# Kernel tuning notes

Measured on AMD Instinct MI355X. Metric: run time of the kernel, lower is better.

The kernel has to match this reference:

```python
import jax, jax.numpy as jnp
import numpy as np

B, T, C = 8, 2048, 1024
E = 8            # num_experts (= world_size in the original)
K = 2            # top-k
CAP_FACTOR = 1.25
CAPACITY = int(T / E * CAP_FACTOR)  # 320, per (expert, batch-row)
DFF = 4 * C


def setup_inputs() -> dict:
    key = jax.random.key(0)
    ks = jax.random.split(key, 4)
    x = jax.random.normal(ks[0], (B, T, C), dtype=jnp.float32)
    Wg = jax.random.normal(ks[1], (C, E), dtype=jnp.float32) * (C ** -0.5)
    bg = jnp.zeros((E,), dtype=jnp.float32)
    W1 = jax.random.normal(ks[2], (E, C, DFF), dtype=jnp.float32) * (C ** -0.5)
    b1 = jnp.zeros((E, DFF), dtype=jnp.float32)
    W2 = jax.random.normal(ks[3], (E, DFF, C), dtype=jnp.float32) * (DFF ** -0.5)
    b2 = jnp.zeros((E, C), dtype=jnp.float32)
    return {"x": x, "Wg": Wg, "bg": bg, "W1": W1, "b1": b1, "W2": W2, "b2": b2}


def reference(x, Wg, bg, W1, b1, W2, b2):
    # Router: linear + softmax, then top-k gating
    probs = jax.nn.softmax(jnp.einsum('btc,ce->bte', x, Wg) + bg, axis=-1)  # [B,T,E]
    topk_p, topk_e = jax.lax.top_k(probs, K)                               # [B,T,K]

    S = T * K  # one "assignment" per (token, k-slot), row-major (t, k) order
    e_flat = topk_e.reshape(B, S)                      # expert id per assignment
    p_flat = topk_p.reshape(B, S)

    # Position of each assignment within its (batch-row, expert) group,
    # ordered by token position then k-slot (matches nonzero() row-major order).
    onehot = (e_flat[..., None] == jnp.arange(E)).astype(jnp.int32)        # [B,S,E]
    pos_all = jnp.cumsum(onehot, axis=1) - 1                                # [B,S,E]
    pos = jnp.take_along_axis(pos_all, e_flat[..., None], axis=2)[..., 0]   # [B,S]
    keep = pos < CAPACITY                               # overflow tokens are dropped

    # Dispatch tokens into padded per-(expert,row) buffers: [E,B,CAPACITY,C]
    x_rep = jnp.repeat(x, K, axis=1)                    # [B,S,C], assignment order
    b_idx = jnp.broadcast_to(jnp.arange(B)[:, None], (B, S))
    pos_scat = jnp.where(keep, pos, CAPACITY)           # out-of-range -> dropped
    dispatch = jnp.zeros((E, B, CAPACITY, C), dtype=x.dtype)
    dispatch = dispatch.at[e_flat, b_idx, pos_scat].set(x_rep, mode='drop')

    # Grouped expert FFN (padding rows are zeros; their outputs are never read back)
    h = jax.nn.relu(jnp.einsum('ebsc,ech->ebsh', dispatch, W1) + b1[:, None, None, :])
    y = jnp.einsum('ebsh,ehc->ebsc', h, W2) + b2[:, None, None, :]

    # Combine: gather back, scale by gate prob (dropped tokens -> padding_val 0)
    gathered = y[e_flat, b_idx, jnp.clip(pos, 0, CAPACITY - 1)]             # [B,S,C]
    out = gathered * jnp.where(keep, p_flat, 0.0)[..., None]
    return out.reshape(B, T, K, C).sum(axis=2)          # sum over k assignments
```

## Files before the change

### kernel.cpp

```cpp
#include <hip/hip_runtime.h>
#include <stdint.h>

#define B_ 8
#define T_ 2048
#define C_ 1024
#define E_ 8
#define K_ 2
#define CAP_ 320
#define DFF_ 4096
#define S_ (T_*K_)
#define NTOK (B_*T_)
#define ROWS_PER_E (B_*CAP_)

typedef __attribute__((ext_vector_type(8))) short short8;
typedef __attribute__((ext_vector_type(4))) float floatx4;

__device__ __forceinline__ unsigned short f2bf(float f) {
  union { float f; unsigned u; } v; v.f = f;
  unsigned r = v.u + 0x7fffu + ((v.u >> 16) & 1u);
  return (unsigned short)(r >> 16);
}
__device__ __forceinline__ float bf2f(unsigned short h) {
  union { unsigned u; float f; } v; v.u = ((unsigned)h) << 16;
  return v.f;
}

#define GLOAD16(g, l) __builtin_amdgcn_global_load_lds( \
    (const __attribute__((address_space(1))) void*)(g), \
    (__attribute__((address_space(3))) void*)(l), 16, 0, 0)

__global__ void router_kernel(const float* __restrict__ x, const float* __restrict__ Wg,
                              const float* __restrict__ bg,
                              int* __restrict__ topk_e, float* __restrict__ topk_p)
{
  int token = (int)((blockIdx.x * blockDim.x + threadIdx.x) >> 6);
  int lane = threadIdx.x & 63;
  if (token >= NTOK) return;
  const float* xr = x + (size_t)token * C_;
  double acc[E_];
  #pragma unroll
  for (int e = 0; e < E_; ++e) acc[e] = 0.0;
  for (int c = lane; c < C_; c += 64) {
    double xv = (double)xr[c];
    const float4* w4 = (const float4*)(Wg + (size_t)c * E_);
    float4 wa = w4[0], wb = w4[1];
    acc[0] += xv * (double)wa.x; acc[1] += xv * (double)wa.y;
    acc[2] += xv * (double)wa.z; acc[3] += xv * (double)wa.w;
    acc[4] += xv * (double)wb.x; acc[5] += xv * (double)wb.y;
    acc[6] += xv * (double)wb.z; acc[7] += xv * (double)wb.w;
  }
  #pragma unroll
  for (int off = 32; off; off >>= 1) {
    #pragma unroll
    for (int e = 0; e < E_; ++e) acc[e] += __shfl_down(acc[e], off, 64);
  }
  if (lane == 0) {
    double lg[E_];
    double mx = -1e300;
    #pragma unroll
    for (int e = 0; e < E_; ++e) { lg[e] = acc[e] + (double)bg[e]; mx = fmax(mx, lg[e]); }
    double se = 0.0, pr[E_];
    #pragma unroll
    for (int e = 0; e < E_; ++e) { pr[e] = exp(lg[e] - mx); se += pr[e]; }
    #pragma unroll
    for (int e = 0; e < E_; ++e) pr[e] /= se;
    int e0 = 0;
    #pragma unroll
    for (int e = 1; e < E_; ++e) if (pr[e] > pr[e0]) e0 = e;
    int e1 = -1;
    #pragma unroll
    for (int e = 0; e < E_; ++e) {
      if (e == e0) continue;
      if (e1 < 0 || pr[e] > pr[e1]) e1 = e;
    }
    topk_e[token*2+0] = e0; topk_p[token*2+0] = (float)pr[e0];
    topk_e[token*2+1] = e1; topk_p[token*2+1] = (float)pr[e1];
  }
}

__global__ void scan_kernel(const int* __restrict__ topk_e,
                            int* __restrict__ pos_arr,
                            int* __restrict__ slot_src,
                            int* __restrict__ counts)
{
  const int b = blockIdx.x;
  const int tid = threadIdx.x;
  const int PT = S_ / 256;
  __shared__ int cnt[256][E_];
  int e_loc[16];
  int local[E_];
  #pragma unroll
  for (int e = 0; e < E_; ++e) local[e] = 0;
  const int* te = topk_e + (size_t)b * S_;
  for (int j = 0; j < PT; ++j) {
    int e = te[tid*PT + j];
    e_loc[j] = e;
    local[e]++;
  }
  #pragma unroll
  for (int e = 0; e < E_; ++e) cnt[tid][e] = local[e];
  __syncthreads();
  if (tid < E_) {
    int run = 0;
    for (int i = 0; i < 256; ++i) { int v = cnt[i][tid]; cnt[i][tid] = run; run += v; }
    counts[tid*B_ + b] = run;
  }
  __syncthreads();
  int base[E_];
  #pragma unroll
  for (int e = 0; e < E_; ++e) base[e] = cnt[tid][e];
  for (int j = 0; j < PT; ++j) {
    int e = e_loc[j];
    int p = base[e]++;
    int s = tid*PT + j;
    if (p < CAP_) {
      pos_arr[(size_t)b*S_ + s] = p;
      slot_src[((size_t)e*B_ + b)*CAP_ + p] = s >> 1;
    } else {
      pos_arr[(size_t)b*S_ + s] = -1;
    }
  }
}

__global__ void transpose_conv_kernel(const float* __restrict__ in, unsigned short* __restrict__ out,
                                      int R, int Cc)
{
  __shared__ float tile[64][33];
  const int e = blockIdx.z;
  const float* ine = in + (size_t)e * R * Cc;
  unsigned short* oute = out + (size_t)e * R * Cc;
  const int c0 = blockIdx.x * 32, r0 = blockIdx.y * 64;
  const int tx = threadIdx.x & 7, ty = threadIdx.x >> 3;
  #pragma unroll
  for (int p = 0; p < 2; ++p) {
    const int rr = p*32 + ty;
    float4 v = *(const float4*)(ine + (size_t)(r0 + rr) * Cc + c0 + tx*4);
    tile[rr][tx*4+0] = v.x; tile[rr][tx*4+1] = v.y;
    tile[rr][tx*4+2] = v.z; tile[rr][tx*4+3] = v.w;
  }
  __syncthreads();
  short8 s;
  #pragma unroll
  for (int j = 0; j < 8; ++j) s[j] = (short)f2bf(tile[tx*8+j][ty]);
  *(short8*)(oute + (size_t)(c0 + ty) * R + r0 + tx*8) = s;
}

__global__ void dispatch_kernel(const float* __restrict__ x, const int* __restrict__ slot_src,
                                const int* __restrict__ counts, unsigned short* __restrict__ Xd,
                                int e_base, int nexp)
{
  int row = (int)((blockIdx.x * blockDim.x + threadIdx.x) >> 6);
  int lane = threadIdx.x & 63;
  int total = nexp * B_ * CAP_;
  if (row >= total) return;
  int el = row / (B_*CAP_);
  int rem = row - el*(B_*CAP_);
  int b = rem / CAP_, slot = rem - b*CAP_;
  int eg = e_base + el;
  int cnt = counts[eg*B_ + b]; if (cnt > CAP_) cnt = CAP_;
  unsigned short* orow = Xd + (size_t)row * C_;
  if (slot < cnt) {
    int t = slot_src[((size_t)eg*B_ + b)*CAP_ + slot];
    const float4* xr = (const float4*)(x + ((size_t)b*T_ + t)*C_);
    #pragma unroll
    for (int i = 0; i < C_/256; ++i) {
      float4 v = xr[i*64 + lane];
      ushort4 o;
      o.x = f2bf(v.x); o.y = f2bf(v.y); o.z = f2bf(v.z); o.w = f2bf(v.w);
      ((ushort4*)orow)[i*64 + lane] = o;
    }
  } else {
    ushort4 z; z.x = z.y = z.z = z.w = 0;
    #pragma unroll
    for (int i = 0; i < C_/256; ++i) ((ushort4*)orow)[i*64 + lane] = z;
  }
}

template<int RELU>
__global__ __launch_bounds__(256, 3) void gemm128_kernel(
    const unsigned short* __restrict__ A,
    const unsigned short* __restrict__ BT,
    const float* __restrict__ bias,
    unsigned short* __restrict__ Out0,
    unsigned short* __restrict__ Out1,
    int M, int N, int Kfull, int klen, int tilesPerSplit, int nwg)
{
  __shared__ __align__(16) unsigned short lds[3*8192];
  const int NT = N >> 7, MT = M >> 7;
  const int bid = blockIdx.x;
  const int wg = (bid & 7) * (nwg >> 3) + (bid >> 3);
  const int sp  = wg / tilesPerSplit;
  const int wgr = wg - sp * tilesPerSplit;
  const int e  = wgr / (MT*NT);
  const int r2 = wgr - e*(MT*NT);
  const int mt = r2 / NT, nt = r2 - mt*NT;
  const int k0 = sp * klen;
  const unsigned short* Ae = A + (size_t)e * M * Kfull;
  const unsigned short* Be = BT + (size_t)e * N * Kfull;
  const float* be = bias ? (bias + (size_t)e * N) : nullptr;
  unsigned short* Oe = (sp == 0 ? Out0 : Out1) + (size_t)e * M * N;
  const int m0 = mt*128, n0 = nt*128;

  const int tid = threadIdx.x, lane = tid & 63, w = tid >> 6;
  const int wr = w >> 1, wc = w & 1;

  floatx4 acc[4][4];
  #pragma unroll
  for (int i = 0; i < 4; ++i)
    #pragma unroll
    for (int j = 0; j < 4; ++j) acc[i][j] = (floatx4){0.f, 0.f, 0.f, 0.f};

  const int c0 = tid, c1 = 256 + tid;
  const int sr0 = c0 >> 2, sr1 = c1 >> 2;
  const int sq0 = ((c0 & 3)*8) ^ (((sr0 >> 1) & 3) << 3);
  const int sq1 = ((c1 & 3)*8) ^ (((sr1 >> 1) & 3) << 3);
  const unsigned short* gA0 = Ae + (size_t)(m0 + sr0)*Kfull + k0 + sq0;
  const unsigned short* gA1 = Ae + (size_t)(m0 + sr1)*Kfull + k0 + sq1;
  const unsigned short* gB0 = Be + (size_t)(n0 + sr0)*Kfull + k0 + sq0;
  const unsigned short* gB1 = Be + (size_t)(n0 + sr1)*Kfull + k0 + sq1;
  const int la0 = w*512, la1 = 2048 + w*512;
  const int lb0 = 4096 + w*512, lb1 = 4096 + 2048 + w*512;

  const int fr = lane & 15, kq = lane >> 4;
  const int aRow = wr*64 + fr;
  const int bRow = wc*64 + fr;
  const int aOff = aRow*32 + ((kq*8) ^ (((aRow >> 1) & 3) << 3));
  const int bOff = 4096 + bRow*32 + ((kq*8) ^ (((bRow >> 1) & 3) << 3));

  const int nk = klen >> 5;

#define STAGE(t, slot) do { \
    GLOAD16(gA0 + (size_t)(t)*32, lds + (slot)*8192 + la0); \
    GLOAD16(gA1 + (size_t)(t)*32, lds + (slot)*8192 + la1); \
    GLOAD16(gB0 + (size_t)(t)*32, lds + (slot)*8192 + lb0); \
    GLOAD16(gB1 + (size_t)(t)*32, lds + (slot)*8192 + lb1); } while(0)

  STAGE(0, 0); STAGE(1, 1);
  asm volatile("s_waitcnt vmcnt(4)" ::: "memory");
  __builtin_amdgcn_s_barrier();

  for (int t = 0; t < nk; ++t) {
    const int slot = t % 3;
    const int ps   = (t + 2) % 3;
    const unsigned short* sT = lds + slot*8192;

    short8 af[4], bf[4];
    #pragma unroll
    for (int mf = 0; mf < 4; ++mf) af[mf] = *(const short8*)(sT + aOff + mf*512);
    #pragma unroll
    for (int nf = 0; nf < 4; ++nf) bf[nf] = *(const short8*)(sT + bOff + nf*512);
    if (t + 2 < nk) STAGE(t+2, ps);

    #pragma unroll
    for (int mf = 0; mf < 4; ++mf)
      #pragma unroll
      for (int nf = 0; nf < 4; ++nf)
        acc[mf][nf] = __builtin_amdgcn_mfma_f32_16x16x32_bf16(af[mf], bf[nf], acc[mf][nf], 0, 0, 0);

    if (t + 1 < nk) {
      asm volatile("s_waitcnt lgkmcnt(0)" ::: "memory");
      if (t + 2 < nk) asm volatile("s_waitcnt vmcnt(4)" ::: "memory");
      else            asm volatile("s_waitcnt vmcnt(0)" ::: "memory");
      __builtin_amdgcn_s_barrier();
    }
  }
#undef STAGE

  const int col = lane & 15, rbase = (lane >> 4) * 4;
  #pragma unroll
  for (int mf = 0; mf < 4; ++mf) {
    const int gr0 = m0 + wr*64 + mf*16 + rbase;
    #pragma unroll
    for (int nf = 0; nf < 4; ++nf) {
      const int gc = n0 + wc*64 + nf*16 + col;
      const float bv = be ? be[gc] : 0.f;
      #pragma unroll
      for (int r = 0; r < 4; ++r) {
        float v = acc[mf][nf][r] + bv;
        if (RELU) v = fmaxf(v, 0.f);
        Oe[(size_t)(gr0 + r)*N + gc] = f2bf(v);
      }
    }
  }
}

__global__ void combine_kernel(const unsigned short* __restrict__ Y0,
                               const unsigned short* __restrict__ Y1,
                               const float* __restrict__ b2c,
                               const int* __restrict__ topk_e, const float* __restrict__ topk_p,
                               const int* __restrict__ pos_arr, float* __restrict__ out)
{
  int token = (int)((blockIdx.x * blockDim.x + threadIdx.x) >> 6);
  int lane = threadIdx.x & 63;
  if (token >= NTOK) return;
  int b = token / T_, t = token - b*T_;
  int s0 = b*S_ + t*2;
  float acc[16];
  #pragma unroll
  for (int i = 0; i < 16; ++i) acc[i] = 0.f;
  #pragma unroll
  for (int k = 0; k < 2; ++k) {
    int pos = pos_arr[s0 + k];
    if (pos < 0) continue;
    int e = topk_e[s0 + k];
    float p = topk_p[s0 + k];
    size_t rowoff = (((size_t)e*B_ + b)*CAP_ + pos) * C_;
    const unsigned short* yr0 = Y0 + rowoff;
    const unsigned short* yr1 = Y1 ? (Y1 + rowoff) : nullptr;
    const float* bb = b2c ? (b2c + (size_t)e * C_) : nullptr;
    #pragma unroll
    for (int i = 0; i < 4; ++i) {
      ushort4 v = ((const ushort4*)yr0)[i*64 + lane];
      float s0v = bf2f(v.x), s1v = bf2f(v.y), s2v = bf2f(v.z), s3v = bf2f(v.w);
      if (yr1) {
        ushort4 u = ((const ushort4*)yr1)[i*64 + lane];
        s0v += bf2f(u.x); s1v += bf2f(u.y); s2v += bf2f(u.z); s3v += bf2f(u.w);
      }
      if (bb) {
        float4 bv = ((const float4*)bb)[i*64 + lane];
        s0v += bv.x; s1v += bv.y; s2v += bv.z; s3v += bv.w;
      }
      acc[i*4+0] += p * s0v;
      acc[i*4+1] += p * s1v;
      acc[i*4+2] += p * s2v;
      acc[i*4+3] += p * s3v;
    }
  }
  float4* orow = (float4*)(out + (size_t)token * C_);
  #pragma unroll
  for (int i = 0; i < 4; ++i) {
    float4 o;
    o.x = acc[i*4+0]; o.y = acc[i*4+1]; o.z = acc[i*4+2]; o.w = acc[i*4+3];
    orow[i*64 + lane] = o;
  }
}

extern "C" void kernel_launch(void* const* d_in, const int* in_sizes, int n_in,
                              void* d_out, int out_size, void* d_ws, size_t ws_size,
                              hipStream_t stream)
{
  const float* x  = (const float*)d_in[0];
  const float* Wg = (const float*)d_in[1];
  const float* bg = (const float*)d_in[2];
  const float* W1 = (const float*)d_in[3];
  const float* b1 = (const float*)d_in[4];
  const float* W2 = (const float*)d_in[5];
  const float* b2 = (const float*)d_in[6];
  float* out = (float*)d_out;

  char* ws = (char*)d_ws;
  size_t off = 0;
  auto alloc = [&](size_t bytes) -> char* {
    char* p = ws + off;
    off = (off + bytes + 255) & ~(size_t)255;
    return p;
  };
  int*   topk_e  = (int*)  alloc((size_t)NTOK * K_ * 4);
  float* topk_p  = (float*)alloc((size_t)NTOK * K_ * 4);
  int*   pos_arr = (int*)  alloc((size_t)B_ * S_ * 4);
  int*   slot_src= (int*)  alloc((size_t)E_ * B_ * CAP_ * 4);
  int*   counts  = (int*)  alloc((size_t)E_ * B_ * 4);
  unsigned short* Ybuf = (unsigned short*)alloc((size_t)E_ * ROWS_PER_E * C_ * 2);
  size_t fixed = off;
  const size_t perE = (size_t)C_ * DFF_ * 2
                    + (size_t)ROWS_PER_E * C_ * 2
                    + (size_t)ROWS_PER_E * DFF_ * 2
                    + 3 * 256;
  int k = 8;
  while (k > 1 && fixed + (size_t)k * perE > ws_size) k >>= 1;
  unsigned short* Wt = (unsigned short*)alloc((size_t)k * C_ * DFF_ * 2);
  unsigned short* Xd = (unsigned short*)alloc((size_t)k * ROWS_PER_E * C_ * 2);
  unsigned short* Hb = (unsigned short*)alloc((size_t)k * ROWS_PER_E * DFF_ * 2);

  router_kernel<<<NTOK/4, 256, 0, stream>>>(x, Wg, bg, topk_e, topk_p);
  scan_kernel<<<B_, 256, 0, stream>>>(topk_e, pos_arr, slot_src, counts);

  const bool splitK2 = (k == 8);

  for (int eb = 0; eb < E_; eb += k) {
    transpose_conv_kernel<<<dim3(DFF_/32, C_/64, k), 256, 0, stream>>>(
        W1 + (size_t)eb * C_ * DFF_, Wt, C_, DFF_);
    dispatch_kernel<<<(k * ROWS_PER_E) / 4, 256, 0, stream>>>(x, slot_src, counts, Xd, eb, k);
    {
      int tiles = k * (ROWS_PER_E/128) * (DFF_/128);
      gemm128_kernel<1><<<tiles, 256, 0, stream>>>(
          Xd, Wt, b1 + (size_t)eb * DFF_, Hb, Hb, ROWS_PER_E, DFF_, C_, C_, tiles, tiles);
    }
    transpose_conv_kernel<<<dim3(C_/32, DFF_/64, k), 256, 0, stream>>>(
        W2 + (size_t)eb * DFF_ * C_, Wt, DFF_, C_);
    {
      int tiles = k * (ROWS_PER_E/128) * (C_/128);
      if (splitK2) {
        gemm128_kernel<0><<<2*tiles, 256, 0, stream>>>(
            Hb, Wt, nullptr, Ybuf, Xd, ROWS_PER_E, C_, DFF_, DFF_/2, tiles, 2*tiles);
      } else {
        gemm128_kernel<0><<<tiles, 256, 0, stream>>>(
            Hb, Wt, b2 + (size_t)eb * C_, Ybuf + (size_t)eb * ROWS_PER_E * C_,
            Ybuf + (size_t)eb * ROWS_PER_E * C_, ROWS_PER_E, C_, DFF_, DFF_, tiles, tiles);
      }
    }
  }

  combine_kernel<<<NTOK/4, 256, 0, stream>>>(
      Ybuf, splitK2 ? Xd : nullptr, splitK2 ? b2 : nullptr,
      topk_e, topk_p, pos_arr, out);
}
```

Baseline: 630.6 us.

## Replace 128x128 GEMM with 256x256 tile, 8-wave kernel and interleaved staging

Replaces the 128x128, 4-wave, triple-buffered GEMM with a 256x256 tile using 8 waves (each computing 128x64), a 64-wide K step split into half-tiles, and A/B loads staggered between four MFMA phases with barriers and s_setprio. Larger tiles raise arithmetic intensity and cut global/LDS traffic per FLOP, and the interleaved schedule aims to overlap loads with MFMA. In exchange it uses 128KB LDS per block (one block per CU) and launches far fewer workgroups: 256x256 tiles give 10x16=160 per expert for GEMM1 and 10x4=40 per expert for GEMM2, which may underfill the CUs for GEMM2. It also adds many barriers per iteration.

```diff
diff --git a/kernel.cpp b/kernel.cpp
--- a/kernel.cpp
+++ b/kernel.cpp
@@ -29,6 +29,8 @@
     (const __attribute__((address_space(1))) void*)(g), \
     (__attribute__((address_space(3))) void*)(l), 16, 0, 0)
 
+#define BARRIER() asm volatile("s_barrier" ::: "memory")
+
 __global__ void router_kernel(const float* __restrict__ x, const float* __restrict__ Wg,
                               const float* __restrict__ bg,
                               int* __restrict__ topk_e, float* __restrict__ topk_p)
@@ -79,8 +81,7 @@
 }
 
 __global__ void scan_kernel(const int* __restrict__ topk_e,
-                            int* __restrict__ pos_arr,
-                            int* __restrict__ slot_src,
+                            int* __restrict__ pos_arr, int* __restrict__ slot_src,
                             int* __restrict__ counts)
 {
   const int b = blockIdx.x;
@@ -177,7 +178,7 @@
 }
 
 template<int RELU>
-__global__ __launch_bounds__(256, 3) void gemm128_kernel(
+__global__ __launch_bounds__(512) void gemm256_kernel(
     const unsigned short* __restrict__ A,
     const unsigned short* __restrict__ BT,
     const float* __restrict__ bias,
@@ -185,8 +186,8 @@
     unsigned short* __restrict__ Out1,
     int M, int N, int Kfull, int klen, int tilesPerSplit, int nwg)
 {
-  __shared__ __align__(16) unsigned short lds[3*8192];
-  const int NT = N >> 7, MT = M >> 7;
+  __shared__ __align__(16) unsigned short lds[65536];
+  const int NT = N >> 8, MT = M >> 8;
   const int bid = blockIdx.x;
   const int wg = (bid & 7) * (nwg >> 3) + (bid >> 3);
   const int sp  = wg / tilesPerSplit;
@@ -199,77 +200,123 @@
   const unsigned short* Be = BT + (size_t)e * N * Kfull;
   const float* be = bias ? (bias + (size_t)e * N) : nullptr;
   unsigned short* Oe = (sp == 0 ? Out0 : Out1) + (size_t)e * M * N;
-  const int m0 = mt*128, n0 = nt*128;
+  const int m0 = mt*256, n0 = nt*256;
 
   const int tid = threadIdx.x, lane = tid & 63, w = tid >> 6;
-  const int wr = w >> 1, wc = w & 1;
-
-  floatx4 acc[4][4];
-  #pragma unroll
-  for (int i = 0; i < 4; ++i)
+  const int wr = w >> 2, wc = w & 3;
+
+  floatx4 acc[8][4];
+  #pragma unroll
+  for (int i = 0; i < 8; ++i)
     #pragma unroll
     for (int j = 0; j < 4; ++j) acc[i][j] = (floatx4){0.f, 0.f, 0.f, 0.f};
 
-  const int c0 = tid, c1 = 256 + tid;
-  const int sr0 = c0 >> 2, sr1 = c1 >> 2;
-  const int sq0 = ((c0 & 3)*8) ^ (((sr0 >> 1) & 3) << 3);
-  const int sq1 = ((c1 & 3)*8) ^ (((sr1 >> 1) & 3) << 3);
-  const unsigned short* gA0 = Ae + (size_t)(m0 + sr0)*Kfull + k0 + sq0;
-  const unsigned short* gA1 = Ae + (size_t)(m0 + sr1)*Kfull + k0 + sq1;
-  const unsigned short* gB0 = Be + (size_t)(n0 + sr0)*Kfull + k0 + sq0;
-  const unsigned short* gB1 = Be + (size_t)(n0 + sr1)*Kfull + k0 + sq1;
-  const int la0 = w*512, la1 = 2048 + w*512;
-  const int lb0 = 4096 + w*512, lb1 = 4096 + 2048 + w*512;
+  const int r0s = tid >> 2;
+  const int p0s = ((tid & 3) ^ (r0s & 3)) * 8;
+  const unsigned short* gA0 = Ae + (size_t)(m0 + r0s)*Kfull + k0 + p0s;
+  const unsigned short* gA1 = gA0 + (size_t)128*Kfull;
+  const unsigned short* gB0 = Be + (size_t)(n0 + r0s)*Kfull + k0 + p0s;
+  const unsigned short* gB1 = gB0 + (size_t)128*Kfull;
+  const int la0 = w*512, la1 = 4096 + w*512;
 
   const int fr = lane & 15, kq = lane >> 4;
-  const int aRow = wr*64 + fr;
-  const int bRow = wc*64 + fr;
-  const int aOff = aRow*32 + ((kq*8) ^ (((aRow >> 1) & 3) << 3));
-  const int bOff = 4096 + bRow*32 + ((kq*8) ^ (((bRow >> 1) & 3) << 3));
-
-  const int nk = klen >> 5;
-
-#define STAGE(t, slot) do { \
-    GLOAD16(gA0 + (size_t)(t)*32, lds + (slot)*8192 + la0); \
-    GLOAD16(gA1 + (size_t)(t)*32, lds + (slot)*8192 + la1); \
-    GLOAD16(gB0 + (size_t)(t)*32, lds + (slot)*8192 + lb0); \
-    GLOAD16(gB1 + (size_t)(t)*32, lds + (slot)*8192 + lb1); } while(0)
-
-  STAGE(0, 0); STAGE(1, 1);
+  const int kqs = ((kq ^ (fr & 3)) * 8);
+  const int aBase = (wr*128 + fr)*32 + kqs;
+  const int bBase = 32768 + (wc*64 + fr)*32 + kqs;
+
+  const int nk = klen >> 6;
+
+#define STAGE_AH(h) do { int _s = (h)&3; size_t _k = (size_t)((h)>>1)*64 + ((h)&1)*32; \
+    GLOAD16(gA0 + _k, lds + _s*8192 + la0); \
+    GLOAD16(gA1 + _k, lds + _s*8192 + la1); } while(0)
+#define STAGE_BH(h) do { int _s = (h)&3; size_t _k = (size_t)((h)>>1)*64 + ((h)&1)*32; \
+    GLOAD16(gB0 + _k, lds + 32768 + _s*8192 + la0); \
+    GLOAD16(gB1 + _k, lds + 32768 + _s*8192 + la1); } while(0)
+
+  STAGE_AH(0); STAGE_BH(0);
+  STAGE_AH(1); STAGE_BH(1);
+  STAGE_AH(2); STAGE_BH(2);
   asm volatile("s_waitcnt vmcnt(4)" ::: "memory");
-  __builtin_amdgcn_s_barrier();
+  BARRIER();
 
   for (int t = 0; t < nk; ++t) {
-    const int slot = t % 3;
-    const int ps   = (t + 2) % 3;
-    const unsigned short* sT = lds + slot*8192;
-
-    short8 af[4], bf[4];
-    #pragma unroll
-    for (int mf = 0; mf < 4; ++mf) af[mf] = *(const short8*)(sT + aOff + mf*512);
-    #pragma unroll
-    for (int nf = 0; nf < 4; ++nf) bf[nf] = *(const short8*)(sT + bOff + nf*512);
-    if (t + 2 < nk) STAGE(t+2, ps);
-
+    const int s0 = (2*t) & 3, s1 = (2*t+1) & 3;
+    const unsigned short* sA0 = lds + s0*8192;
+    const unsigned short* sA1 = lds + s1*8192;
+    short8 af[4], bfr[4];
+
+    #pragma unroll
+    for (int nf = 0; nf < 4; ++nf) bfr[nf] = *(const short8*)(sA0 + bBase + nf*512);
+    #pragma unroll
+    for (int mf = 0; mf < 4; ++mf) af[mf] = *(const short8*)(sA0 + aBase + mf*512);
+    if (t + 1 < nk) STAGE_AH(2*(t+1)+1);
+    BARRIER();
+    asm volatile("s_waitcnt lgkmcnt(0)" ::: "memory");
+    __builtin_amdgcn_s_setprio(1);
     #pragma unroll
     for (int mf = 0; mf < 4; ++mf)
       #pragma unroll
       for (int nf = 0; nf < 4; ++nf)
-        acc[mf][nf] = __builtin_amdgcn_mfma_f32_16x16x32_bf16(af[mf], bf[nf], acc[mf][nf], 0, 0, 0);
+        acc[mf][nf] = __builtin_amdgcn_mfma_f32_16x16x32_bf16(af[mf], bfr[nf], acc[mf][nf], 0, 0, 0);
+    __builtin_amdgcn_s_setprio(0);
+    BARRIER();
+
+    #pragma unroll
+    for (int mf = 0; mf < 4; ++mf) af[mf] = *(const short8*)(sA0 + aBase + (mf+4)*512);
+    if (t + 1 < nk) STAGE_BH(2*(t+1)+1);
+    BARRIER();
+    asm volatile("s_waitcnt lgkmcnt(0)" ::: "memory");
+    __builtin_amdgcn_s_setprio(1);
+    #pragma unroll
+    for (int mf = 0; mf < 4; ++mf)
+      #pragma unroll
+      for (int nf = 0; nf < 4; ++nf)
+        acc[mf+4][nf] = __builtin_amdgcn_mfma_f32_16x16x32_bf16(af[mf], bfr[nf], acc[mf+4][nf], 0, 0, 0);
+    __builtin_amdgcn_s_setprio(0);
+    BARRIER();
+
+    #pragma unroll
+    for (int nf = 0; nf < 4; ++nf) bfr[nf] = *(const short8*)(sA1 + bBase + nf*512);
+    #pragma unroll
+    for (int mf = 0; mf < 4; ++mf) af[mf] = *(const short8*)(sA1 + aBase + mf*512);
+    if (t + 2 < nk) STAGE_AH(2*(t+2));
+    BARRIER();
+    asm volatile("s_waitcnt lgkmcnt(0)" ::: "memory");
+    __builtin_amdgcn_s_setprio(1);
+    #pragma unroll
+    for (int mf = 0; mf < 4; ++mf)
+      #pragma unroll
+      for (int nf = 0; nf < 4; ++nf)
+        acc[mf][nf] = __builtin_amdgcn_mfma_f32_16x16x32_bf16(af[mf], bfr[nf], acc[mf][nf], 0, 0, 0);
+    __builtin_amdgcn_s_setprio(0);
+    BARRIER();
+
+    #pragma unroll
+    for (int mf = 0; mf < 4; ++mf) af[mf] = *(const short8*)(sA1 + aBase + (mf+4)*512);
+    if (t + 2 < nk) STAGE_BH(2*(t+2));
+    BARRIER();
+    asm volatile("s_waitcnt lgkmcnt(0)" ::: "memory");
+    __builtin_amdgcn_s_setprio(1);
+    #pragma unroll
+    for (int mf = 0; mf < 4; ++mf)
+      #pragma unroll
+      for (int nf = 0; nf < 4; ++nf)
+        acc[mf+4][nf] = __builtin_amdgcn_mfma_f32_16x16x32_bf16(af[mf], bfr[nf], acc[mf+4][nf], 0, 0, 0);
+    __builtin_amdgcn_s_setprio(0);
 
     if (t + 1 < nk) {
-      asm volatile("s_waitcnt lgkmcnt(0)" ::: "memory");
       if (t + 2 < nk) asm volatile("s_waitcnt vmcnt(4)" ::: "memory");
       else            asm volatile("s_waitcnt vmcnt(0)" ::: "memory");
-      __builtin_amdgcn_s_barrier();
-    }
-  }
-#undef STAGE
+      BARRIER();
+    }
+  }
+#undef STAGE_AH
+#undef STAGE_BH
 
   const int col = lane & 15, rbase = (lane >> 4) * 4;
   #pragma unroll
-  for (int mf = 0; mf < 4; ++mf) {
-    const int gr0 = m0 + wr*64 + mf*16 + rbase;
+  for (int mf = 0; mf < 8; ++mf) {
+    const int gr0 = m0 + wr*128 + mf*16 + rbase;
     #pragma unroll
     for (int nf = 0; nf < 4; ++nf) {
       const int gc = n0 + wc*64 + nf*16 + col;
@@ -382,19 +429,19 @@
         W1 + (size_t)eb * C_ * DFF_, Wt, C_, DFF_);
     dispatch_kernel<<<(k * ROWS_PER_E) / 4, 256, 0, stream>>>(x, slot_src, counts, Xd, eb, k);
     {
-      int tiles = k * (ROWS_PER_E/128) * (DFF_/128);
-      gemm128_kernel<1><<<tiles, 256, 0, stream>>>(
+      int tiles = k * (ROWS_PER_E/256) * (DFF_/256);
+      gemm256_kernel<1><<<tiles, 512, 0, stream>>>(
           Xd, Wt, b1 + (size_t)eb * DFF_, Hb, Hb, ROWS_PER_E, DFF_, C_, C_, tiles, tiles);
     }
     transpose_conv_kernel<<<dim3(C_/32, DFF_/64, k), 256, 0, stream>>>(
         W2 + (size_t)eb * DFF_ * C_, Wt, DFF_, C_);
     {
-      int tiles = k * (ROWS_PER_E/128) * (C_/128);
+      int tiles = k * (ROWS_PER_E/256) * (C_/256);
       if (splitK2) {
-        gemm128_kernel<0><<<2*tiles, 256, 0, stream>>>(
+        gemm256_kernel<0><<<2*tiles, 512, 0, stream>>>(
             Hb, Wt, nullptr, Ybuf, Xd, ROWS_PER_E, C_, DFF_, DFF_/2, tiles, 2*tiles);
       } else {
-        gemm128_kernel<0><<<tiles, 256, 0, stream>>>(
+        gemm256_kernel<0><<<tiles, 512, 0, stream>>>(
             Hb, Wt, b2 + (size_t)eb * C_, Ybuf + (size_t)eb * ROWS_PER_E * C_,
             Ybuf + (size_t)eb * ROWS_PER_E * C_, ROWS_PER_E, C_, DFF_, DFF_, tiles, tiles);
       }
```

After: 595.9 us. 1.06x faster.
